# Kernel tuning notes

Hardware: AMD Instinct MI355X
Metric: run time of the kernel (lower is better)

## Reference

```python
import jax, jax.numpy as jnp
from jax import lax
import numpy as np

K_TOP = 100
NMS_THRESH = 0.5
SUBJECT_CATEGORY_ID = 0


def box_cxcywh_to_xyxy(b):
    cx, cy, w, h = b[..., 0], b[..., 1], b[..., 2], b[..., 3]
    return jnp.stack([cx - 0.5 * w, cy - 0.5 * h, cx + 0.5 * w, cy + 0.5 * h], axis=-1)


def _pairwise_iou(boxes):
    # boxes: [K,4] xyxy; uses the +1 pixel convention from the original numpy NMS
    x1, y1, x2, y2 = boxes[:, 0], boxes[:, 1], boxes[:, 2], boxes[:, 3]
    area = (x2 - x1 + 1.0) * (y2 - y1 + 1.0)
    xx1 = jnp.maximum(x1[:, None], x1[None, :])
    yy1 = jnp.maximum(y1[:, None], y1[None, :])
    xx2 = jnp.minimum(x2[:, None], x2[None, :])
    yy2 = jnp.minimum(y2[:, None], y2[None, :])
    w = jnp.maximum(0.0, xx2 - xx1 + 1.0)
    h = jnp.maximum(0.0, yy2 - yy1 + 1.0)
    inter = w * h
    union = area[:, None] + area[None, :] - inter
    return inter / union


def _nms_keep(sub_boxes, obj_boxes, obj_labels, hoi_scores):
    # Greedy grouped pairwise NMS for one image.
    # Grouping key degenerates to object label (subject cat and verb-row are constant).
    K = sub_boxes.shape[0]
    max_scores = hoi_scores.max(axis=-1)
    order = jnp.argsort(-max_scores)
    ovr = _pairwise_iou(sub_boxes) * _pairwise_iou(obj_boxes)  # [K,K]
    same_group = obj_labels[:, None] == obj_labels[None, :]
    ovr = jnp.where(same_group, ovr, 0.0)
    ovr_s = ovr[order][:, order]
    upper = jnp.triu(jnp.ones((K, K), dtype=bool), k=1)
    sup_mat = (ovr_s > NMS_THRESH) & upper  # suppression only of later (lower-score) items

    def body(i, st):
        suppressed, keep = st
        ki = jnp.logical_not(suppressed[i])
        keep = keep.at[i].set(ki)
        suppressed = suppressed | (ki & sup_mat[i])
        return suppressed, keep

    _, keep_sorted = lax.fori_loop(0, K, body, (jnp.zeros(K, bool), jnp.zeros(K, bool)))
    return jnp.zeros(K, bool).at[order].set(keep_sorted)


def setup_inputs() -> dict:
    key = jax.random.key(0)
    k1, k2, k3, k4, k5, k6 = jax.random.split(key, 6)
    B, Q, C, V = 256, 300, 81, 117
    return {
        "pred_obj_logits": jax.random.normal(k1, (B, Q, C), dtype=jnp.float32),
        "pred_verb_logits": jax.random.normal(k2, (B, Q, V), dtype=jnp.float32),
        "pred_sub_boxes": jax.random.uniform(k3, (B, Q, 4), dtype=jnp.float32),
        "pred_obj_boxes": jax.random.uniform(k4, (B, Q, 4), dtype=jnp.float32),
        "correct_mat": (jax.random.uniform(k5, (V, C), dtype=jnp.float32) > 0.3).astype(jnp.float32),
        "target_sizes": jax.random.randint(k6, (B, 2), 200, 640, dtype=jnp.int32),
    }


def reference(pred_obj_logits, pred_verb_logits, pred_sub_boxes, pred_obj_boxes, correct_mat, target_sizes):
    B, Q, C = pred_obj_logits.shape
    V = pred_verb_logits.shape[-1]

    obj_prob = jax.nn.softmax(pred_obj_logits, axis=-1)       # [B,Q,C]  (no_obj=False)
    verb_scores = jax.nn.sigmoid(pred_verb_logits)            # [B,Q,V]

    topk_values, topk_indexes = lax.top_k(obj_prob.reshape(B, Q * C), K_TOP)  # [B,100]
    topk_boxes = topk_indexes // C
    obj_labels = topk_indexes % C

    vs = jnp.take_along_axis(verb_scores, topk_boxes[..., None], axis=1)      # [B,100,V]
    ob = jnp.take_along_axis(pred_obj_boxes, topk_boxes[..., None], axis=1)   # [B,100,4]
    sb = jnp.take_along_axis(pred_sub_boxes, topk_boxes[..., None], axis=1)

    img_h = target_sizes[:, 0].astype(jnp.float32)
    img_w = target_sizes[:, 1].astype(jnp.float32)
    scale_fct = jnp.stack([img_w, img_h, img_w, img_h], axis=1)  # [B,4]
    sub_boxes = box_cxcywh_to_xyxy(sb) * scale_fct[:, None, :]
    obj_boxes = box_cxcywh_to_xyxy(ob) * scale_fct[:, None, :]

    hoi_scores = vs * topk_values[..., None]                    # [B,100,V]
    # masks[b,k,v] = correct_mat[v, obj_labels[b,k]]
    masks = correct_mat.T[obj_labels]                           # [B,100,V]
    hoi_scores = hoi_scores * masks

    keep = jax.vmap(_nms_keep)(sub_boxes, obj_boxes, obj_labels, hoi_scores)  # [B,100] bool
    final_scores = hoi_scores * keep[..., None].astype(hoi_scores.dtype)

    return final_scores, topk_values, obj_labels, sub_boxes, obj_boxes, keep
```

## Files before the change

kernel.cpp:

```cpp
#include <hip/hip_runtime.h>
#include <cmath>

#pragma clang fp contract(off)

#define NT 1024
constexpr int B_ = 256, Q_ = 300, C_ = 81, V_ = 117, K_ = 100;
constexpr int QC_ = Q_ * C_;
constexpr int KV_ = K_ * V_;
constexpr int NB  = 2048;
constexpr int CAP = 1024;

using u32 = unsigned int;
using u64 = unsigned long long;
using u16 = unsigned short;
using u8  = unsigned char;

constexpr int OFF_P16  = 0;
constexpr int OFF_HIST = 48600;
constexpr int OFF_RMAX = OFF_HIST + 8192;
constexpr int OFF_RINV = OFF_RMAX + 1200;
constexpr int OFF_BSUB = OFF_RINV + 1200;
constexpr int OFF_BOBJ = OFF_BSUB + 1600;
constexpr int OFF_SUPR = OFF_BOBJ + 1600;
constexpr int OFF_SELV = OFF_SUPR + 1600;
constexpr int OFF_SELI = OFF_SELV + 400;
constexpr int OFF_MAXB = OFF_SELI + 400;
constexpr int OFF_ORD  = OFF_MAXB + 400;
constexpr int OFF_MISC = OFF_ORD + 104;
constexpr int SMEM_SZ  = OFF_MISC + 48;
static_assert(SMEM_SZ <= 65536, "LDS overflow");

__device__ __forceinline__ u64 shfl_xor_u64(u64 v, int mask) {
    u32 lo = (u32)v, hi = (u32)(v >> 32);
    lo = (u32)__shfl_xor((int)lo, mask, 64);
    hi = (u32)__shfl_xor((int)hi, mask, 64);
    return ((u64)hi << 32) | lo;
}

__device__ __forceinline__ float iou1(const float* a, const float* b) {
    float areaA = (a[2] - a[0] + 1.f) * (a[3] - a[1] + 1.f);
    float areaB = (b[2] - b[0] + 1.f) * (b[3] - b[1] + 1.f);
    float xx1 = fmaxf(a[0], b[0]);
    float yy1 = fmaxf(a[1], b[1]);
    float xx2 = fminf(a[2], b[2]);
    float yy2 = fminf(a[3], b[3]);
    float w = fmaxf(0.f, xx2 - xx1 + 1.f);
    float h = fmaxf(0.f, yy2 - yy1 + 1.f);
    float inter = w * h;
    return inter / (areaA + areaB - inter);
}

__global__ __launch_bounds__(NT) void hoi_kernel(
    const float* __restrict__ obj_logits,
    const float* __restrict__ verb_logits,
    const float* __restrict__ sub_boxes_in,
    const float* __restrict__ obj_boxes_in,
    const float* __restrict__ cm,
    const int*   __restrict__ tsizes,
    float* __restrict__ out)
{
    const int b = blockIdx.x;
    const int tid = threadIdx.x;

    __shared__ __align__(16) u8 smem[SMEM_SZ];
    u16*   p16     = (u16*)(smem + OFF_P16);
    float* hs      = (float*)(smem + OFF_P16);
    u32*   hist    = (u32*)(smem + OFF_HIST);
    u64*   cand    = (u64*)(smem + OFF_HIST);
    float* rowmax  = (float*)(smem + OFF_RMAX);
    float* rinv    = (float*)(smem + OFF_RINV);
    float (*bsub)[4]   = (float(*)[4])(smem + OFF_BSUB);
    float (*bobj)[4]   = (float(*)[4])(smem + OFF_BOBJ);
    u32   (*suprow)[4] = (u32(*)[4])(smem + OFF_SUPR);
    float* sel_val = (float*)(smem + OFF_SELV);
    u32*   sel_idx = (u32*)(smem + OFF_SELI);
    u32*   maxbits = (u32*)(smem + OFF_MAXB);
    u8*    order8  = (u8*)(smem + OFF_ORD);
    u32*   skeep     = (u32*)(smem + OFF_MISC);
    u32*   keep_bits = (u32*)(smem + OFF_MISC + 16);
    u32*   s_cnt     = (u32*)(smem + OFF_MISC + 32);
    int*   sT        = (int*)(smem + OFF_MISC + 36);
    int*   sW        = (int*)(smem + OFF_MISC + 40);
    u32*   sAcc      = (u32*)(smem + OFF_MISC + 44);
    u32*   swsum   = (u32*)(smem + OFF_BSUB);
    u64*   wred    = (u64*)(smem + OFF_BOBJ);
    u64*   s_prev  = (u64*)(smem + OFF_SUPR);

    const float* lg = obj_logits + (size_t)b * QC_;

    for (int i = tid; i < NB; i += NT) hist[i] = 0;
    if (tid == 0) *s_cnt = 0;
    __syncthreads();

    {
        int g = tid >> 5, l = tid & 31;
        bool have2 = (l < C_ - 64);
        for (int q = g; q < Q_; q += 32) {
            const float* row = lg + q * C_;
            float v0 = row[l], v1 = row[l + 32];
            float v2 = have2 ? row[l + 64] : -INFINITY;
            float m = fmaxf(fmaxf(v0, v1), v2);
            for (int off = 16; off; off >>= 1) m = fmaxf(m, __shfl_xor(m, off, 64));
            float e0 = expf(v0 - m), e1 = expf(v1 - m);
            float e2 = have2 ? expf(v2 - m) : 0.f;
            float s = e0 + e1 + e2;
            for (int off = 16; off; off >>= 1) s += __shfl_xor(s, off, 64);
            float ri = 1.f / s;
            float p0 = e0 * ri, p1 = e1 * ri;
            u32 b0 = __float_as_uint(p0), b1 = __float_as_uint(p1);
            p16[q * C_ + l]      = (u16)(b0 >> 16);
            p16[q * C_ + l + 32] = (u16)(b1 >> 16);
            atomicAdd(&hist[b0 >> 21], 1u);
            atomicAdd(&hist[b1 >> 21], 1u);
            if (have2) {
                float p2 = e2 * ri;
                u32 b2 = __float_as_uint(p2);
                p16[q * C_ + l + 64] = (u16)(b2 >> 16);
                atomicAdd(&hist[b2 >> 21], 1u);
            }
            if (l == 0) { rowmax[q] = m; rinv[q] = ri; }
        }
    }
    __syncthreads();

    u32 my_c, my_suf;
    {
        int t = tid;
        my_c = hist[2 * t] + hist[2 * t + 1];
        my_suf = my_c;
        #pragma unroll
        for (int off = 1; off < 64; off <<= 1) {
            u32 o = (u32)__shfl_down((int)my_suf, off, 64);
            my_suf += ((tid & 63) + off < 64) ? o : 0;
        }
        if ((tid & 63) == 0) swsum[tid >> 6] = my_suf;
    }
    __syncthreads();
    if (tid < 16) {
        u32 sufW = swsum[tid];
        #pragma unroll
        for (int off = 1; off < 16; off <<= 1) {
            u32 o = (u32)__shfl_down((int)sufW, off, 64);
            sufW += (tid + off < 16) ? o : 0;
        }
        u32 nxt = (u32)__shfl_down((int)sufW, 1, 64);
        if (tid == 15) nxt = 0;
        if (sufW >= (u32)K_ && nxt < (u32)K_) { *sW = tid; *sAcc = nxt; }
    }
    __syncthreads();
    if ((tid >> 6) == *sW) {
        u32 above = *sAcc + (my_suf - my_c);
        if (above < (u32)K_ && above + my_c >= (u32)K_) {
            u32 acc = above + hist[2 * tid + 1];
            *sT = (acc >= (u32)K_) ? (2 * tid + 1) : (2 * tid);
        }
    }
    __syncthreads();
    const int T = *sT;
    __syncthreads();

    for (int i = tid; i < QC_; i += NT) {
        u32 pb = p16[i];
        if ((int)(pb >> 5) >= T) {
            u32 pos = atomicAdd(s_cnt, 1u);
            if (pos < (u32)CAP) {
                int q = i / C_;
                float p = expf(lg[i] - rowmax[q]) * rinv[q];
                cand[pos] = ((u64)__float_as_uint(p) << 32) | (u32)(~i);
            }
        }
    }
    __syncthreads();
    const int ncand = (int)*s_cnt;

    auto cswap = [](u64& a, u64& bb, bool up) {
        if ((a > bb) == up) { u64 t = a; a = bb; bb = t; }
    };

    if (ncand <= 256) {
        if (tid < 64) {
            u64 v0 = (tid < ncand) ? cand[tid] : 0ull;
            u64 v1 = (64 + tid < ncand) ? cand[64 + tid] : 0ull;
            u64 v2 = (128 + tid < ncand) ? cand[128 + tid] : 0ull;
            u64 v3 = (192 + tid < ncand) ? cand[192 + tid] : 0ull;
            for (int k = 2; k <= 256; k <<= 1) {
                for (int j = k >> 1; j > 0; j >>= 1) {
                    if (j == 128) {
                        cswap(v0, v2, true);
                        cswap(v1, v3, true);
                    } else if (j == 64) {
                        cswap(v0, v1, true);
                        cswap(v2, v3, (k == 256));
                    } else {
                        auto step = [&](u64& v, int ebase) {
                            u64 pv = shfl_xor_u64(v, j);
                            int e = ebase + tid;
                            bool up = ((e & k) == 0);
                            bool lower = ((e & j) == 0);
                            u64 mn = v < pv ? v : pv;
                            u64 mx = v < pv ? pv : v;
                            v = (lower == up) ? mn : mx;
                        };
                        step(v0, 0); step(v1, 64); step(v2, 128); step(v3, 192);
                    }
                }
            }
            int e2 = 128 + tid;
            if (e2 >= 156) {
                int t = 255 - e2;
                sel_val[t] = __uint_as_float((u32)(v2 >> 32));
                sel_idx[t] = ~(u32)v2;
            }
            int t3 = 255 - (192 + tid);
            sel_val[t3] = __uint_as_float((u32)(v3 >> 32));
            sel_idx[t3] = ~(u32)v3;
        }
    } else if (ncand <= CAP) {
        for (int e = tid; e < CAP; e += NT)
            if (e >= ncand) cand[e] = 0;
        __syncthreads();
        for (int k = 2; k <= CAP; k <<= 1) {
            for (int j = k >> 1; j > 0; j >>= 1) {
                int e = tid, partner = e ^ j;
                if (partner > e) {
                    u64 a = cand[e], bb = cand[partner];
                    bool up = ((e & k) == 0);
                    if ((a > bb) == up) { cand[e] = bb; cand[partner] = a; }
                }
                __syncthreads();
            }
        }
        if (tid < K_) {
            u64 m = cand[CAP - 1 - tid];
            sel_val[tid] = __uint_as_float((u32)(m >> 32));
            sel_idx[tid] = ~(u32)m;
        }
    } else {
        if (tid == 0) *s_prev = ~0ull;
        __syncthreads();
        for (int r = 0; r < K_; r++) {
            u64 prev = *s_prev;
            u64 local = 0;
            for (int i = tid; i < QC_; i += NT) {
                int q = i / C_;
                float p = expf(lg[i] - rowmax[q]) * rinv[q];
                u64 key = ((u64)__float_as_uint(p) << 32) | (u32)(~i);
                if (key < prev && key > local) local = key;
            }
            for (int off = 32; off > 0; off >>= 1) {
                u64 o = shfl_xor_u64(local, off);
                if (o > local) local = o;
            }
            if ((tid & 63) == 0) wred[tid >> 6] = local;
            __syncthreads();
            if (tid == 0) {
                u64 m = wred[0];
                for (int wv = 1; wv < 16; wv++) if (wred[wv] > m) m = wred[wv];
                *s_prev = m;
                u32 idx = ~(u32)m;
                if (idx >= (u32)QC_) idx = 0;
                sel_val[r] = __uint_as_float((u32)(m >> 32));
                sel_idx[r] = idx;
            }
            __syncthreads();
        }
    }
    __syncthreads();

    if (tid < K_) {
        int idx = (int)sel_idx[tid];
        int q = idx / C_;
        float iw = (float)tsizes[b * 2 + 1];
        float ih = (float)tsizes[b * 2 + 0];
        float4 sb = ((const float4*)sub_boxes_in)[(size_t)b * Q_ + q];
        float4 ob = ((const float4*)obj_boxes_in)[(size_t)b * Q_ + q];
        bsub[tid][0] = (sb.x - 0.5f * sb.z) * iw; bsub[tid][1] = (sb.y - 0.5f * sb.w) * ih;
        bsub[tid][2] = (sb.x + 0.5f * sb.z) * iw; bsub[tid][3] = (sb.y + 0.5f * sb.w) * ih;
        bobj[tid][0] = (ob.x - 0.5f * ob.z) * iw; bobj[tid][1] = (ob.y - 0.5f * ob.w) * ih;
        bobj[tid][2] = (ob.x + 0.5f * ob.z) * iw; bobj[tid][3] = (ob.y + 0.5f * ob.w) * ih;
        suprow[tid][0] = 0; suprow[tid][1] = 0; suprow[tid][2] = 0; suprow[tid][3] = 0;
    }
    if (tid >= 128 && tid < 132) keep_bits[tid - 128] = 0;
    __syncthreads();

    for (int f = tid; f < KV_; f += NT) {
        int r = f / V_, v = f - r * V_;
        int idx = (int)sel_idx[r];
        int q = idx / C_, lab = idx - q * C_;
        float x = verb_logits[((size_t)b * Q_ + q) * V_ + v];
        float s = 1.f / (1.f + expf(-x));
        hs[f] = s * sel_val[r] * cm[v * C_ + lab];
    }
    __syncthreads();

    if (tid < 800) {
        int r = tid >> 3, j = tid & 7;
        float m = 0.f;
        for (int k = 0; k < 15; k++) {
            int v = j * 15 + k;
            if (v < V_) m = fmaxf(m, hs[r * V_ + v]);
        }
        for (int off = 4; off; off >>= 1) m = fmaxf(m, __shfl_xor(m, off, 64));
        if (j == 0) maxbits[r] = __float_as_uint(m);
    }
    __syncthreads();

    if (tid < 800) {
        int r = tid >> 3, j = tid & 7;
        u64 kr = ((u64)maxbits[r] << 32) | (u32)(~r);
        int rank = 0;
        for (int k = 0; k < 13; k++) {
            int jj = j * 13 + k;
            if (jj < K_) {
                u64 kj = ((u64)maxbits[jj] << 32) | (u32)(~jj);
                rank += (kj > kr) ? 1 : 0;
            }
        }
        for (int off = 4; off; off >>= 1) rank += __shfl_xor(rank, off, 64);
        if (j == 0) order8[rank] = (u8)r;
    }
    __syncthreads();

    for (int e = tid; e < K_ * K_; e += NT) {
        int i = e / K_, j = e - i * K_;
        if (j > i) {
            int ri = order8[i], rj = order8[j];
            u32 li = sel_idx[ri] % (u32)C_, lj = sel_idx[rj] % (u32)C_;
            if (li == lj) {
                float o = iou1(bsub[ri], bsub[rj]) * iou1(bobj[ri], bobj[rj]);
                if (o > 0.5f)
                    atomicOr(&suprow[i][j >> 5], 1u << (j & 31));
            }
        }
    }
    __syncthreads();

    if (tid < 64) {
        u32 ra0 = suprow[tid][0], ra1 = suprow[tid][1], ra2 = suprow[tid][2], ra3 = suprow[tid][3];
        u32 rb0 = 0, rb1 = 0, rb2 = 0, rb3 = 0;
        if (tid < K_ - 64) {
            rb0 = suprow[tid + 64][0]; rb1 = suprow[tid + 64][1];
            rb2 = suprow[tid + 64][2]; rb3 = suprow[tid + 64][3];
        }
        u32 acc[4] = {0, 0, 0, 0};
        u32 km[4]  = {0, 0, 0, 0};
        #pragma unroll
        for (int i = 0; i < K_; i++) {
            u32 r0, r1, r2, r3;
            if (i < 64) {
                r0 = (u32)__shfl((int)ra0, i, 64); r1 = (u32)__shfl((int)ra1, i, 64);
                r2 = (u32)__shfl((int)ra2, i, 64); r3 = (u32)__shfl((int)ra3, i, 64);
            } else {
                r0 = (u32)__shfl((int)rb0, i - 64, 64); r1 = (u32)__shfl((int)rb1, i - 64, 64);
                r2 = (u32)__shfl((int)rb2, i - 64, 64); r3 = (u32)__shfl((int)rb3, i - 64, 64);
            }
            bool sup_i = (acc[i >> 5] >> (i & 31)) & 1u;
            if (!sup_i) {
                km[i >> 5] |= 1u << (i & 31);
                acc[0] |= r0; acc[1] |= r1; acc[2] |= r2; acc[3] |= r3;
            }
        }
        if (tid == 0) { skeep[0] = km[0]; skeep[1] = km[1]; skeep[2] = km[2]; skeep[3] = km[3]; }
    }
    __syncthreads();
    if (tid < K_) {
        if ((skeep[tid >> 5] >> (tid & 31)) & 1u) {
            int r = order8[tid];
            atomicOr(&keep_bits[r >> 5], 1u << (r & 31));
        }
    }
    __syncthreads();

    float* o0 = out;
    float* o1 = out + (size_t)B_ * KV_;
    float* o2 = o1 + (size_t)B_ * K_;
    float* o3 = o2 + (size_t)B_ * K_;
    float* o4 = o3 + (size_t)B_ * K_ * 4;
    float* o5 = o4 + (size_t)B_ * K_ * 4;

    for (int f = tid; f < KV_; f += NT) {
        int r = f / V_;
        bool kp = (keep_bits[r >> 5] >> (r & 31)) & 1u;
        o0[(size_t)b * KV_ + f] = kp ? hs[f] : 0.f;
    }
    if (tid < K_) {
        bool kp = (keep_bits[tid >> 5] >> (tid & 31)) & 1u;
        o1[(size_t)b * K_ + tid] = sel_val[tid];
        o2[(size_t)b * K_ + tid] = (float)(sel_idx[tid] % (u32)C_);
        o5[(size_t)b * K_ + tid] = kp ? 1.f : 0.f;
    }
    if (tid < K_ * 4) {
        int r = tid >> 2, k = tid & 3;
        o3[((size_t)b * K_) * 4 + tid] = bsub[r][k];
        o4[((size_t)b * K_) * 4 + tid] = bobj[r][k];
    }
}

extern "C" void kernel_launch(void* const* d_in, const int* in_sizes, int n_in,
                              void* d_out, int out_size, void* d_ws, size_t ws_size,
                              hipStream_t stream) {
    const float* obj_logits  = (const float*)d_in[0];
    const float* verb_logits = (const float*)d_in[1];
    const float* sub_boxes   = (const float*)d_in[2];
    const float* obj_boxes   = (const float*)d_in[3];
    const float* cm          = (const float*)d_in[4];
    const int*   ts          = (const int*)d_in[5];
    hipLaunchKernelGGL(hoi_kernel, dim3(B_), dim3(NT), 0, stream,
                       obj_logits, verb_logits, sub_boxes, obj_boxes, cm, ts,
                       (float*)d_out);
}
```

Baseline: 145.4 us.

## Unroll softmax rows, vectorize LDS scans, precompute box areas, float4 output stores

Softmax now handles two rows per warp-group per iteration so the shuffle reductions of both rows can interleave. The candidate scan reads two packed u16s at once. Box setup is split across three thread ranges, and per-box areas are precomputed into LDS so the IoU code loads boxes as float4 and skips recomputing areas. The verb-score loop is unrolled by two, and the masked score output is written with float4 stores. This adds register pressure and relies on the new 16-byte alignment of the box arrays and of the output offset.

```diff
diff --git a/kernel.cpp b/kernel.cpp
--- a/kernel.cpp
+++ b/kernel.cpp
@@ -19,7 +19,7 @@
 constexpr int OFF_HIST = 48600;
 constexpr int OFF_RMAX = OFF_HIST + 8192;
 constexpr int OFF_RINV = OFF_RMAX + 1200;
-constexpr int OFF_BSUB = OFF_RINV + 1200;
+constexpr int OFF_BSUB = OFF_RINV + 1208;
 constexpr int OFF_BOBJ = OFF_BSUB + 1600;
 constexpr int OFF_SUPR = OFF_BOBJ + 1600;
 constexpr int OFF_SELV = OFF_SUPR + 1600;
@@ -29,6 +29,7 @@
 constexpr int OFF_MISC = OFF_ORD + 104;
 constexpr int SMEM_SZ  = OFF_MISC + 48;
 static_assert(SMEM_SZ <= 65536, "LDS overflow");
+static_assert((OFF_BSUB & 15) == 0 && (OFF_BOBJ & 15) == 0, "b128 align");
 
 __device__ __forceinline__ u64 shfl_xor_u64(u64 v, int mask) {
     u32 lo = (u32)v, hi = (u32)(v >> 32);
@@ -37,17 +38,15 @@
     return ((u64)hi << 32) | lo;
 }
 
-__device__ __forceinline__ float iou1(const float* a, const float* b) {
-    float areaA = (a[2] - a[0] + 1.f) * (a[3] - a[1] + 1.f);
-    float areaB = (b[2] - b[0] + 1.f) * (b[3] - b[1] + 1.f);
-    float xx1 = fmaxf(a[0], b[0]);
-    float yy1 = fmaxf(a[1], b[1]);
-    float xx2 = fminf(a[2], b[2]);
-    float yy2 = fminf(a[3], b[3]);
+__device__ __forceinline__ float iou4(float4 a, float4 b, float areaSum) {
+    float xx1 = fmaxf(a.x, b.x);
+    float yy1 = fmaxf(a.y, b.y);
+    float xx2 = fminf(a.z, b.z);
+    float yy2 = fminf(a.w, b.w);
     float w = fmaxf(0.f, xx2 - xx1 + 1.f);
     float h = fmaxf(0.f, yy2 - yy1 + 1.f);
     float inter = w * h;
-    return inter / (areaA + areaB - inter);
+    return inter / (areaSum - inter);
 }
 
 __global__ __launch_bounds__(NT) void hoi_kernel(
@@ -67,6 +66,8 @@
     float* hs      = (float*)(smem + OFF_P16);
     u32*   hist    = (u32*)(smem + OFF_HIST);
     u64*   cand    = (u64*)(smem + OFF_HIST);
+    float* asub    = (float*)(smem + OFF_HIST);
+    float* aobj    = (float*)(smem + OFF_HIST + 512);
     float* rowmax  = (float*)(smem + OFF_RMAX);
     float* rinv    = (float*)(smem + OFF_RINV);
     float (*bsub)[4]   = (float(*)[4])(smem + OFF_BSUB);
@@ -95,30 +96,65 @@
     {
         int g = tid >> 5, l = tid & 31;
         bool have2 = (l < C_ - 64);
-        for (int q = g; q < Q_; q += 32) {
-            const float* row = lg + q * C_;
-            float v0 = row[l], v1 = row[l + 32];
-            float v2 = have2 ? row[l + 64] : -INFINITY;
-            float m = fmaxf(fmaxf(v0, v1), v2);
-            for (int off = 16; off; off >>= 1) m = fmaxf(m, __shfl_xor(m, off, 64));
-            float e0 = expf(v0 - m), e1 = expf(v1 - m);
-            float e2 = have2 ? expf(v2 - m) : 0.f;
-            float s = e0 + e1 + e2;
-            for (int off = 16; off; off >>= 1) s += __shfl_xor(s, off, 64);
-            float ri = 1.f / s;
-            float p0 = e0 * ri, p1 = e1 * ri;
-            u32 b0 = __float_as_uint(p0), b1 = __float_as_uint(p1);
-            p16[q * C_ + l]      = (u16)(b0 >> 16);
-            p16[q * C_ + l + 32] = (u16)(b1 >> 16);
-            atomicAdd(&hist[b0 >> 21], 1u);
-            atomicAdd(&hist[b1 >> 21], 1u);
-            if (have2) {
-                float p2 = e2 * ri;
-                u32 b2 = __float_as_uint(p2);
-                p16[q * C_ + l + 64] = (u16)(b2 >> 16);
-                atomicAdd(&hist[b2 >> 21], 1u);
-            }
-            if (l == 0) { rowmax[q] = m; rinv[q] = ri; }
+        for (int q = g; q < Q_; q += 64) {
+            int qB = q + 32;
+            bool hasB = (qB < Q_);
+            const float* rowA = lg + q * C_;
+            const float* rowB = lg + (hasB ? qB : q) * C_;
+            float a0 = rowA[l], a1 = rowA[l + 32];
+            float b0 = rowB[l], b1 = rowB[l + 32];
+            float a2 = have2 ? rowA[l + 64] : -INFINITY;
+            float b2 = have2 ? rowB[l + 64] : -INFINITY;
+            float mA = fmaxf(fmaxf(a0, a1), a2);
+            float mB = fmaxf(fmaxf(b0, b1), b2);
+            #pragma unroll
+            for (int off = 16; off; off >>= 1) {
+                mA = fmaxf(mA, __shfl_xor(mA, off, 64));
+                mB = fmaxf(mB, __shfl_xor(mB, off, 64));
+            }
+            float eA0 = expf(a0 - mA), eA1 = expf(a1 - mA);
+            float eB0 = expf(b0 - mB), eB1 = expf(b1 - mB);
+            float eA2 = have2 ? expf(a2 - mA) : 0.f;
+            float eB2 = have2 ? expf(b2 - mB) : 0.f;
+            float sA = eA0 + eA1 + eA2;
+            float sB = eB0 + eB1 + eB2;
+            #pragma unroll
+            for (int off = 16; off; off >>= 1) {
+                sA += __shfl_xor(sA, off, 64);
+                sB += __shfl_xor(sB, off, 64);
+            }
+            float riA = 1.f / sA;
+            float riB = 1.f / sB;
+            {
+                float p0 = eA0 * riA, p1 = eA1 * riA;
+                u32 x0 = __float_as_uint(p0), x1 = __float_as_uint(p1);
+                p16[q * C_ + l]      = (u16)(x0 >> 16);
+                p16[q * C_ + l + 32] = (u16)(x1 >> 16);
+                atomicAdd(&hist[x0 >> 21], 1u);
+                atomicAdd(&hist[x1 >> 21], 1u);
+                if (have2) {
+                    float p2 = eA2 * riA;
+                    u32 x2 = __float_as_uint(p2);
+                    p16[q * C_ + l + 64] = (u16)(x2 >> 16);
+                    atomicAdd(&hist[x2 >> 21], 1u);
+                }
+                if (l == 0) { rowmax[q] = mA; rinv[q] = riA; }
+            }
+            if (hasB) {
+                float p0 = eB0 * riB, p1 = eB1 * riB;
+                u32 x0 = __float_as_uint(p0), x1 = __float_as_uint(p1);
+                p16[qB * C_ + l]      = (u16)(x0 >> 16);
+                p16[qB * C_ + l + 32] = (u16)(x1 >> 16);
+                atomicAdd(&hist[x0 >> 21], 1u);
+                atomicAdd(&hist[x1 >> 21], 1u);
+                if (have2) {
+                    float p2 = eB2 * riB;
+                    u32 x2 = __float_as_uint(p2);
+                    p16[qB * C_ + l + 64] = (u16)(x2 >> 16);
+                    atomicAdd(&hist[x2 >> 21], 1u);
+                }
+                if (l == 0) { rowmax[qB] = mB; rinv[qB] = riB; }
+            }
         }
     }
     __syncthreads();
@@ -159,11 +195,22 @@
     const int T = *sT;
     __syncthreads();
 
-    for (int i = tid; i < QC_; i += NT) {
-        u32 pb = p16[i];
-        if ((int)(pb >> 5) >= T) {
+    for (int i0 = tid * 2; i0 < QC_; i0 += 2 * NT) {
+        u32 two = *(const u32*)(p16 + i0);
+        u32 pb0 = two & 0xFFFFu, pb1 = two >> 16;
+        if ((int)(pb0 >> 5) >= T) {
             u32 pos = atomicAdd(s_cnt, 1u);
             if (pos < (u32)CAP) {
+                int i = i0;
+                int q = i / C_;
+                float p = expf(lg[i] - rowmax[q]) * rinv[q];
+                cand[pos] = ((u64)__float_as_uint(p) << 32) | (u32)(~i);
+            }
+        }
+        if ((int)(pb1 >> 5) >= T) {
+            u32 pos = atomicAdd(s_cnt, 1u);
+            if (pos < (u32)CAP) {
+                int i = i0 + 1;
                 int q = i / C_;
                 float p = expf(lg[i] - rowmax[q]) * rinv[q];
                 cand[pos] = ((u64)__float_as_uint(p) << 32) | (u32)(~i);
@@ -273,23 +320,47 @@
         float iw = (float)tsizes[b * 2 + 1];
         float ih = (float)tsizes[b * 2 + 0];
         float4 sb = ((const float4*)sub_boxes_in)[(size_t)b * Q_ + q];
+        float x1 = (sb.x - 0.5f * sb.z) * iw, y1 = (sb.y - 0.5f * sb.w) * ih;
+        float x2 = (sb.x + 0.5f * sb.z) * iw, y2 = (sb.y + 0.5f * sb.w) * ih;
+        bsub[tid][0] = x1; bsub[tid][1] = y1; bsub[tid][2] = x2; bsub[tid][3] = y2;
+        asub[tid] = (x2 - x1 + 1.f) * (y2 - y1 + 1.f);
+    } else if (tid >= 128 && tid < 128 + K_) {
+        int t = tid - 128;
+        int idx = (int)sel_idx[t];
+        int q = idx / C_;
+        float iw = (float)tsizes[b * 2 + 1];
+        float ih = (float)tsizes[b * 2 + 0];
         float4 ob = ((const float4*)obj_boxes_in)[(size_t)b * Q_ + q];
-        bsub[tid][0] = (sb.x - 0.5f * sb.z) * iw; bsub[tid][1] = (sb.y - 0.5f * sb.w) * ih;
-        bsub[tid][2] = (sb.x + 0.5f * sb.z) * iw; bsub[tid][3] = (sb.y + 0.5f * sb.w) * ih;
-        bobj[tid][0] = (ob.x - 0.5f * ob.z) * iw; bobj[tid][1] = (ob.y - 0.5f * ob.w) * ih;
-        bobj[tid][2] = (ob.x + 0.5f * ob.z) * iw; bobj[tid][3] = (ob.y + 0.5f * ob.w) * ih;
-        suprow[tid][0] = 0; suprow[tid][1] = 0; suprow[tid][2] = 0; suprow[tid][3] = 0;
-    }
-    if (tid >= 128 && tid < 132) keep_bits[tid - 128] = 0;
-    __syncthreads();
-
-    for (int f = tid; f < KV_; f += NT) {
-        int r = f / V_, v = f - r * V_;
-        int idx = (int)sel_idx[r];
-        int q = idx / C_, lab = idx - q * C_;
-        float x = verb_logits[((size_t)b * Q_ + q) * V_ + v];
-        float s = 1.f / (1.f + expf(-x));
-        hs[f] = s * sel_val[r] * cm[v * C_ + lab];
+        float x1 = (ob.x - 0.5f * ob.z) * iw, y1 = (ob.y - 0.5f * ob.w) * ih;
+        float x2 = (ob.x + 0.5f * ob.z) * iw, y2 = (ob.y + 0.5f * ob.w) * ih;
+        bobj[t][0] = x1; bobj[t][1] = y1; bobj[t][2] = x2; bobj[t][3] = y2;
+        aobj[t] = (x2 - x1 + 1.f) * (y2 - y1 + 1.f);
+    } else if (tid >= 256 && tid < 256 + K_) {
+        int t = tid - 256;
+        suprow[t][0] = 0; suprow[t][1] = 0; suprow[t][2] = 0; suprow[t][3] = 0;
+    } else if (tid >= 384 && tid < 388) {
+        keep_bits[tid - 384] = 0;
+    }
+    __syncthreads();
+
+    for (int f = tid; f < KV_; f += 2 * NT) {
+        int fB = f + NT;
+        bool hB = (fB < KV_);
+        int fB2 = hB ? fB : f;
+        int rA = f / V_,  vA = f - rA * V_;
+        int rB = fB2 / V_, vB = fB2 - rB * V_;
+        u32 idxA = sel_idx[rA], idxB = sel_idx[rB];
+        int qA = (int)idxA / C_, labA = (int)idxA - qA * C_;
+        int qB = (int)idxB / C_, labB = (int)idxB - qB * C_;
+        float xA = verb_logits[((size_t)b * Q_ + qA) * V_ + vA];
+        float xB = verb_logits[((size_t)b * Q_ + qB) * V_ + vB];
+        float cA = cm[vA * C_ + labA];
+        float cB = cm[vB * C_ + labB];
+        float svA = sel_val[rA], svB = sel_val[rB];
+        float sgA = 1.f / (1.f + expf(-xA));
+        float sgB = 1.f / (1.f + expf(-xB));
+        hs[f] = sgA * svA * cA;
+        if (hB) hs[fB] = sgB * svB * cB;
     }
     __syncthreads();
 
@@ -327,7 +398,12 @@
             int ri = order8[i], rj = order8[j];
             u32 li = sel_idx[ri] % (u32)C_, lj = sel_idx[rj] % (u32)C_;
             if (li == lj) {
-                float o = iou1(bsub[ri], bsub[rj]) * iou1(bobj[ri], bobj[rj]);
+                float4 s_i = *(const float4*)bsub[ri];
+                float4 s_j = *(const float4*)bsub[rj];
+                float4 b_i = *(const float4*)bobj[ri];
+                float4 b_j = *(const float4*)bobj[rj];
+                float o = iou4(s_i, s_j, asub[ri] + asub[rj]) *
+                          iou4(b_i, b_j, aobj[ri] + aobj[rj]);
                 if (o > 0.5f)
                     atomicOr(&suprow[i][j >> 5], 1u << (j & 31));
             }
@@ -378,10 +454,20 @@
     float* o4 = o3 + (size_t)B_ * K_ * 4;
     float* o5 = o4 + (size_t)B_ * K_ * 4;
 
-    for (int f = tid; f < KV_; f += NT) {
-        int r = f / V_;
-        bool kp = (keep_bits[r >> 5] >> (r & 31)) & 1u;
-        o0[(size_t)b * KV_ + f] = kp ? hs[f] : 0.f;
+    constexpr int KV4_ = KV_ / 4;
+    for (int f4 = tid; f4 < KV4_; f4 += NT) {
+        int base = f4 * 4;
+        float4 h = *(const float4*)(hs + base);
+        int r0 = base / V_, m0 = base - r0 * V_;
+        int r1 = r0 + ((m0 + 1) >= V_ ? 1 : 0);
+        int r2 = r0 + ((m0 + 2) >= V_ ? 1 : 0);
+        int r3 = r0 + ((m0 + 3) >= V_ ? 1 : 0);
+        float4 o;
+        o.x = ((keep_bits[r0 >> 5] >> (r0 & 31)) & 1u) ? h.x : 0.f;
+        o.y = ((keep_bits[r1 >> 5] >> (r1 & 31)) & 1u) ? h.y : 0.f;
+        o.z = ((keep_bits[r2 >> 5] >> (r2 & 31)) & 1u) ? h.z : 0.f;
+        o.w = ((keep_bits[r3 >> 5] >> (r3 & 31)) & 1u) ? h.w : 0.f;
+        *(float4*)(o0 + (size_t)b * KV_ + base) = o;
     }
     if (tid < K_) {
         bool kp = (keep_bits[tid >> 5] >> (tid & 31)) & 1u;
```

Measured after the change: 144.2 us. Within noise of the previous version (-0.9%).
